# Performance work log

Measured on AMD Instinct MI355X. Metric: run time of the kernel, lower is better.

## Reference

```python
import jax, jax.numpy as jnp
import numpy as np

B, N, C = 2, 4096, 512
NUM_HEADS = 8
HEAD_DIM = C // NUM_HEADS
SCALE = HEAD_DIM ** -0.5
THETA = 10000.0


def setup_inputs() -> dict:
    key = jax.random.key(0)
    ks = jax.random.split(key, 5)
    x = jax.random.normal(ks[0], (B, N, C), dtype=jnp.float32)
    Wqkv = jax.random.normal(ks[1], (3 * C, C), dtype=jnp.float32) * 0.02
    bqkv = jax.random.normal(ks[2], (3 * C,), dtype=jnp.float32) * 0.02
    Wproj = jax.random.normal(ks[3], (C, C), dtype=jnp.float32) * 0.02
    bproj = jax.random.normal(ks[4], (C,), dtype=jnp.float32) * 0.02
    return {"x": x, "Wqkv": Wqkv, "bqkv": bqkv, "Wproj": Wproj, "bproj": bproj}


def _rope(x, seq_len, head_dim):
    # x: [B, H, N, head_dim]; interleaved rotary embedding
    freqs = 1.0 / THETA ** (jnp.arange(0, head_dim, 2, dtype=jnp.float32) / head_dim)  # [hd/2]
    t = jnp.arange(seq_len, dtype=jnp.float32)
    freqs_cis = jnp.outer(t, freqs)                      # [N, hd/2]
    sin_f = jnp.sin(freqs_cis)
    cos_f = jnp.cos(freqs_cis)
    x_even = x[..., ::2]                                 # [B, H, N, hd/2]
    x_odd = x[..., 1::2]
    rot = jnp.stack(
        [x_even * cos_f - x_odd * sin_f,
         x_even * sin_f + x_odd * cos_f],
        axis=-1,
    )                                                    # [B, H, N, hd/2, 2]
    return rot.reshape(x.shape)


def reference(x, Wqkv, bqkv, Wproj, bproj):
    b, n, c = x.shape
    # fused QKV projection: y = x @ W.T + b
    qkv = x @ Wqkv.T + bqkv                              # [B, N, 3C]
    qkv = qkv.reshape(b, n, 3, NUM_HEADS, HEAD_DIM)
    qkv = jnp.transpose(qkv, (2, 0, 3, 1, 4))            # [3, B, H, N, hd]
    q, k, v = qkv[0], qkv[1], qkv[2]
    q = _rope(q, n, HEAD_DIM)
    k = _rope(k, n, HEAD_DIM)
    attn = jnp.einsum('bhqd,bhkd->bhqk', q, k) * SCALE   # [B, H, N, N]
    attn = jax.nn.softmax(attn, axis=-1)
    out = jnp.einsum('bhqk,bhkd->bhqd', attn, v)         # [B, H, N, hd]
    out = jnp.transpose(out, (0, 2, 1, 3)).reshape(b, n, c)
    return out @ Wproj.T + bproj
```

## Files before the change

### kernel.cpp

```cpp
#include <hip/hip_runtime.h>
#include <hip/hip_bf16.h>
#include <stdint.h>

#define B_ 2
#define N_ 4096
#define C_ 512
#define H_ 8
#define D_ 64
#define M_ (B_*N_)
#define K3_ (3*C_)
#define NCH 2

typedef __attribute__((ext_vector_type(8)))  short short8;
typedef __attribute__((ext_vector_type(4)))  float f32x4;
typedef __attribute__((ext_vector_type(16))) float f32x16;

static __device__ __forceinline__ unsigned short f2bf(float f) {
  union { float f; unsigned u; } cv; cv.f = f;
  unsigned r = cv.u + 0x7fffu + ((cv.u >> 16) & 1u);
  return (unsigned short)(r >> 16);
}
static __device__ __forceinline__ float bf2f(short x) {
  union { unsigned u; float f; } cv;
  cv.u = ((unsigned)(unsigned short)x) << 16;
  return cv.f;
}
static __device__ __forceinline__ float fexp2(float x) {
#if __has_builtin(__builtin_amdgcn_exp2f)
  return __builtin_amdgcn_exp2f(x);
#else
  return exp2f(x);
#endif
}
static __device__ __forceinline__ unsigned cvt_pk_bf16(float a, float b) {
  unsigned r;
  asm("v_cvt_pk_bf16_f32 %0, %1, %2" : "=v"(r) : "v"(a), "v"(b));
  return r;
}
static __device__ __forceinline__ void gload_lds16(const void* g, void* l) {
  __builtin_amdgcn_global_load_lds((const __attribute__((address_space(1))) unsigned*)g,
                                   (__attribute__((address_space(3))) unsigned*)l, 16, 0, 0);
}
static __device__ __forceinline__ f32x16 zero16() {
  f32x16 z;
#pragma unroll
  for (int i = 0; i < 16; i++) z[i] = 0.f;
  return z;
}

__global__ void prep(const float* __restrict__ x, const float* __restrict__ Wqkv,
                     const float* __restrict__ Wproj,
                     short* __restrict__ xb, short* __restrict__ wqkvb,
                     short* __restrict__ wprjb, float2* __restrict__ tab) {
  int blk = blockIdx.x, t = threadIdx.x;
  if (blk < 4096) {
    int i = blk * 256 + t;
    float4 v = ((const float4*)x)[i];
    short4 o;
    o.x = (short)f2bf(v.x); o.y = (short)f2bf(v.y);
    o.z = (short)f2bf(v.z); o.w = (short)f2bf(v.w);
    ((short4*)xb)[i] = o;
  } else if (blk < 4864) {
    int i = (blk - 4096) * 256 + t;
    float4 v = ((const float4*)Wqkv)[i];
    short4 o;
    o.x = (short)f2bf(v.x); o.y = (short)f2bf(v.y);
    o.z = (short)f2bf(v.z); o.w = (short)f2bf(v.w);
    ((short4*)wqkvb)[i] = o;
  } else if (blk < 5120) {
    int i = (blk - 4864) * 256 + t;
    float4 v = ((const float4*)Wproj)[i];
    short4 o;
    o.x = (short)f2bf(v.x); o.y = (short)f2bf(v.y);
    o.z = (short)f2bf(v.z); o.w = (short)f2bf(v.w);
    ((short4*)wprjb)[i] = o;
  } else {
    int i = (blk - 5120) * 256 + t;
    int p = i & 31, n = i >> 5;
    float freq = exp2f(-((float)(2 * p) / 64.0f) * 13.287712379549449f);
    float ang = (float)n * freq;
    float s, c;
    sincosf(ang, &s, &c);
    float2 r; r.x = c; r.y = s;
    tab[i] = r;
  }
}

__global__ void rope_vt(const short* __restrict__ qkvb, const float2* __restrict__ tab,
                        short* __restrict__ Qf, short* __restrict__ Kf,
                        short* __restrict__ Vf) {
  __shared__ short tile[128][72];
  int blk = blockIdx.x, t = threadIdx.x;
  if (blk < 1024) {
    int tk = blk >> 9;
    int bh = (blk & 511) >> 5;
    int nb4 = blk & 31;
    int b = bh >> 3, h = bh & 7;
    int n0 = nb4 * 128;
#pragma unroll
    for (int pass = 0; pass < 4; pass++) {
      int row = pass * 32 + (t >> 3), chunk = t & 7;
      short8 v = *(const short8*)(qkvb + (size_t)(b * N_ + n0 + row) * K3_ + tk * C_ + h * D_ + chunk * 8);
      *(short8*)&tile[row][chunk * 8] = v;
    }
    __syncthreads();
    int lane = t & 63, f = t >> 6;
    int c = lane & 31, hi = lane >> 5;
    int d0 = f * 16 + hi * 8;
    float sc = (tk == 0) ? 0.18033688011112042f : 1.0f;
    short* base = (tk ? Kf : Qf);
#pragma unroll
    for (int i = 0; i < 4; i++) {
      int n_l = i * 32 + c;
      short8 v = *(const short8*)&tile[n_l][d0];
      const float2* tp = tab + (size_t)(n0 + n_l) * 32 + (d0 >> 1);
      short8 w;
#pragma unroll
      for (int j = 0; j < 4; j++) {
        float e = bf2f(v[2 * j]), o = bf2f(v[2 * j + 1]);
        float2 cs = tp[j];
        float e2 = (e * cs.x - o * cs.y) * sc;
        float o2 = (e * cs.y + o * cs.x) * sc;
        w[2 * j] = (short)f2bf(e2);
        w[2 * j + 1] = (short)f2bf(o2);
      }
      short* dst = base + (((size_t)(bh * 128 + nb4 * 4 + i) * 4 + f) * 512) + lane * 8;
      *(short8*)dst = w;
    }
  } else {
    int blk2 = blk - 1024;
    int bh = blk2 >> 7, kblk = blk2 & 127;
    int b = bh >> 3, h = bh & 7;
    int n0 = kblk * 32;
    {
      int row = t >> 3, c8 = t & 7;
      short8 v = *(const short8*)(qkvb + (size_t)(b * N_ + n0 + row) * K3_ + 2 * C_ + h * D_ + c8 * 8);
      *(short8*)&tile[row][c8 * 8] = v;
    }
    __syncthreads();
    {
      int frag = t >> 6, lane = t & 63;
      int hi = lane >> 5, c = lane & 31;
      int g = frag & 1, dblk = frag >> 1;
      short8 w;
#pragma unroll
      for (int j = 0; j < 8; j++) w[j] = tile[g * 16 + hi * 8 + j][dblk * 32 + c];
      *(short8*)(Vf + ((size_t)(bh * 128 + kblk) * 4 + frag) * 512 + lane * 8) = w;
    }
  }
}

template<int OUTF32>
__global__ __launch_bounds__(256) void gemm_bt(const short* __restrict__ A, const short* __restrict__ Bw,
                                               const float* __restrict__ bias, void* __restrict__ Cout,
                                               int M, int Nout, int K) {
  __shared__ short As[128 * 32];
  __shared__ short Bs[128 * 32];
  int t = threadIdx.x, lane = t & 63, w = t >> 6, wr = w >> 1, wc = w & 1;
  int tM = blockIdx.x * 128, tN = blockIdx.y * 128;
  int lrow = lane & 15, lhi = lane >> 4;
  f32x4 acc[4][4];
#pragma unroll
  for (int fm = 0; fm < 4; fm++)
#pragma unroll
    for (int fn = 0; fn < 4; fn++)
#pragma unroll
      for (int r = 0; r < 4; r++) acc[fm][fn][r] = 0.f;

  int srow = t >> 2, sq = (t & 3) * 8;
  const short* Ag0 = A  + (size_t)(tM + srow) * K + sq;
  const short* Ag1 = A  + (size_t)(tM + 64 + srow) * K + sq;
  const short* Bg0 = Bw + (size_t)(tN + srow) * K + sq;
  const short* Bg1 = Bw + (size_t)(tN + 64 + srow) * K + sq;
  short* Al0 = As + t * 8;          short* Al1 = As + 2048 + t * 8;
  short* Bl0 = Bs + t * 8;          short* Bl1 = Bs + 2048 + t * 8;

  for (int k0 = 0; k0 < K; k0 += 32) {
    gload_lds16(Ag0 + k0, Al0);
    gload_lds16(Ag1 + k0, Al1);
    gload_lds16(Bg0 + k0, Bl0);
    gload_lds16(Bg1 + k0, Bl1);
    __syncthreads();
    short8 af[4], bfr[4];
#pragma unroll
    for (int f = 0; f < 4; f++) {
      af[f]  = *(const short8*)(As + (wr * 64 + f * 16 + lrow) * 32 + lhi * 8);
      bfr[f] = *(const short8*)(Bs + (wc * 64 + f * 16 + lrow) * 32 + lhi * 8);
    }
#pragma unroll
    for (int fm = 0; fm < 4; fm++)
#pragma unroll
      for (int fn = 0; fn < 4; fn++)
        acc[fm][fn] = __builtin_amdgcn_mfma_f32_16x16x32_bf16(af[fm], bfr[fn], acc[fm][fn], 0, 0, 0);
    __syncthreads();
  }

#pragma unroll
  for (int fn = 0; fn < 4; fn++) {
    int col = tN + wc * 64 + fn * 16 + lrow;
    float bv = bias[col];
#pragma unroll
    for (int fm = 0; fm < 4; fm++) {
      int row0 = tM + wr * 64 + fm * 16 + lhi * 4;
#pragma unroll
      for (int r = 0; r < 4; r++) {
        float v = acc[fm][fn][r] + bv;
        if (OUTF32) ((float*)Cout)[(size_t)(row0 + r) * Nout + col] = v;
        else        ((short*)Cout)[(size_t)(row0 + r) * Nout + col] = (short)f2bf(v);
      }
    }
  }
}

static __device__ __forceinline__ void ld4(short8* dst, const short* p) {
#pragma unroll
  for (int f = 0; f < 4; f++) dst[f] = *(const short8*)(p + f * 512);
}
static __device__ __forceinline__ f32x16 qk4(const short8* k, const short8* q, const f32x16& z0) {
  __builtin_amdgcn_s_setprio(1);
  f32x16 st = __builtin_amdgcn_mfma_f32_32x32x16_bf16(k[0], q[0], z0, 0, 0, 0);
  st = __builtin_amdgcn_mfma_f32_32x32x16_bf16(k[1], q[1], st, 0, 0, 0);
  st = __builtin_amdgcn_mfma_f32_32x32x16_bf16(k[2], q[2], st, 0, 0, 0);
  st = __builtin_amdgcn_mfma_f32_32x32x16_bf16(k[3], q[3], st, 0, 0, 0);
  __builtin_amdgcn_s_setprio(0);
  return st;
}
static __device__ __forceinline__ void soft_pv(const f32x16& st, const short8* v,
                                               f32x16& o0, f32x16& o1, float& lsum) {
  float ls = 0.f;
  unsigned cpk[8];
#pragma unroll
  for (int q2 = 0; q2 < 4; q2++) {
    float e0 = fexp2(st[4 * q2]),     e1 = fexp2(st[4 * q2 + 1]);
    float e2 = fexp2(st[4 * q2 + 2]), e3 = fexp2(st[4 * q2 + 3]);
    ls += (e0 + e1) + (e2 + e3);
    cpk[2 * q2]     = cvt_pk_bf16(e0, e1);
    cpk[2 * q2 + 1] = cvt_pk_bf16(e2, e3);
  }
  lsum += ls;
  unsigned w00 = cpk[0], w02 = cpk[2];
  asm volatile("v_permlane32_swap_b32 %0, %1" : "+v"(w00), "+v"(w02));
  unsigned w01 = cpk[1], w03 = cpk[3];
  asm volatile("v_permlane32_swap_b32 %0, %1" : "+v"(w01), "+v"(w03));
  unsigned w10 = cpk[4], w12 = cpk[6];
  asm volatile("v_permlane32_swap_b32 %0, %1" : "+v"(w10), "+v"(w12));
  unsigned w11 = cpk[5], w13 = cpk[7];
  asm volatile("v_permlane32_swap_b32 %0, %1" : "+v"(w11), "+v"(w13));
  union { unsigned u[4]; short8 s; } u0, u1;
  u0.u[0] = w00; u0.u[1] = w01; u0.u[2] = w02; u0.u[3] = w03;
  u1.u[0] = w10; u1.u[1] = w11; u1.u[2] = w12; u1.u[3] = w13;
  __builtin_amdgcn_s_setprio(1);
  o0 = __builtin_amdgcn_mfma_f32_32x32x16_bf16(u0.s, v[0], o0, 0, 0, 0);
  o0 = __builtin_amdgcn_mfma_f32_32x32x16_bf16(u1.s, v[1], o0, 0, 0, 0);
  o1 = __builtin_amdgcn_mfma_f32_32x32x16_bf16(u0.s, v[2], o1, 0, 0, 0);
  o1 = __builtin_amdgcn_mfma_f32_32x32x16_bf16(u1.s, v[3], o1, 0, 0, 0);
  __builtin_amdgcn_s_setprio(0);
}

__global__ __launch_bounds__(256, 4) void attn(const short* __restrict__ Qf, const short* __restrict__ Kf,
                                               const short* __restrict__ Vf,
                                               short* __restrict__ Op, float* __restrict__ lp) {
  __shared__ short Ks[2][2048];
  __shared__ short Vs[2][2048];
  int bh = blockIdx.x;
  int ch = blockIdx.z;
  int t = threadIdx.x;
  int wv = t >> 6, lane = t & 63;
  int c = lane & 31, hi = lane >> 5;
  int q0 = blockIdx.y * 128 + wv * 32;
  const int nkb = N_ / (NCH * 32);
  int kb0 = ch * nkb;

  const short* Qb = Qf + ((size_t)(bh * 128 + (q0 >> 5)) * 4) * 512 + lane * 8;
  const short* Kg = Kf + ((size_t)(bh * 128 + kb0) * 4) * 512 + t * 8;
  const short* Vg = Vf + ((size_t)(bh * 128 + kb0) * 4) * 512 + t * 8;

  short8 qf4[4];
  ld4(qf4, Qb);

  const f32x16 z0 = zero16();
  f32x16 o0 = z0, o1 = z0;
  float lsum = 0.f;

  gload_lds16(Kg, &Ks[0][t * 8]);
  gload_lds16(Vg, &Vs[0][t * 8]);
  __syncthreads();

  int buf = 0;
  for (int it = 0; it < nkb; ++it) {
    if (it + 1 < nkb) {
      gload_lds16(Kg + (size_t)(it + 1) * 2048, &Ks[buf ^ 1][t * 8]);
      gload_lds16(Vg + (size_t)(it + 1) * 2048, &Vs[buf ^ 1][t * 8]);
    }
    short8 kf[4], vf[4];
#pragma unroll
    for (int f = 0; f < 4; f++) kf[f] = *(const short8*)&Ks[buf][f * 512 + lane * 8];
#pragma unroll
    for (int f = 0; f < 4; f++) vf[f] = *(const short8*)&Vs[buf][f * 512 + lane * 8];
    f32x16 st = qk4(kf, qf4, z0);
    soft_pv(st, vf, o0, o1, lsum);
    __syncthreads();
    buf ^= 1;
  }

  float lt = lsum + __shfl_xor(lsum, 32);
  if (hi == 0) lp[((size_t)ch * 16 + bh) * N_ + q0 + c] = lt;
  short* obase = Op + ((size_t)ch * 16 + bh) * N_ * D_;
#pragma unroll
  for (int r = 0; r < 16; r++) {
    int ql = (r & 3) + 8 * (r >> 2) + 4 * hi;
    int n = q0 + ql;
    obase[(size_t)n * D_ + c]      = (short)f2bf(o0[r]);
    obase[(size_t)n * D_ + 32 + c] = (short)f2bf(o1[r]);
  }
}

__global__ void combine(const short* __restrict__ Op, const float* __restrict__ lp,
                        short* __restrict__ AO) {
  int i = blockIdx.x * blockDim.x + threadIdx.x;
  if (i >= 16 * N_ * 8) return;
  int d8 = i & 7, q = (i >> 3) & (N_ - 1), bh = i >> 15;
  const size_t chs = (size_t)16 * N_ * D_;
  size_t base = ((size_t)bh * N_ + q) * D_ + d8 * 8;
  float acc[8];
#pragma unroll
  for (int j = 0; j < 8; j++) acc[j] = 0.f;
  float l = 0.f;
#pragma unroll
  for (int chv = 0; chv < NCH; chv++) {
    short8 v = *(const short8*)(Op + chv * chs + base);
#pragma unroll
    for (int j = 0; j < 8; j++) acc[j] += bf2f(v[j]);
    l += lp[((size_t)chv * 16 + bh) * N_ + q];
  }
  float inv = 1.0f / l;
  int bb = bh >> 3, h = bh & 7;
  short8 o;
#pragma unroll
  for (int j = 0; j < 8; j++) o[j] = (short)f2bf(acc[j] * inv);
  *(short8*)(AO + ((size_t)(bb * N_ + q)) * C_ + h * D_ + d8 * 8) = o;
}

extern "C" void kernel_launch(void* const* d_in, const int* in_sizes, int n_in,
                              void* d_out, int out_size, void* d_ws, size_t ws_size,
                              hipStream_t stream) {
  const float* x     = (const float*)d_in[0];
  const float* Wqkv  = (const float*)d_in[1];
  const float* bqkv  = (const float*)d_in[2];
  const float* Wproj = (const float*)d_in[3];
  const float* bproj = (const float*)d_in[4];
  float* out = (float*)d_out;
  char* ws = (char*)d_ws;

  const size_t off_wprjb = 0;
  const size_t off_tab   = 524288;
  const size_t off_q     = 1572864;
  const size_t off_k     = 9961472;
  const size_t off_vt    = 18350080;
  const size_t off_ao    = 26738688;
  const size_t off_xb    = 35127296;
  const size_t off_wqkvb = 43515904;
  const size_t off_qkvb  = 45088768;
  const size_t off_op    = 35127296;
  const size_t off_l     = 68681728;
  if (ws_size < 70254592) return;

  short* xb    = (short*)(ws + off_xb);
  short* wqkvb = (short*)(ws + off_wqkvb);
  short* wprjb = (short*)(ws + off_wprjb);
  short* qkvb  = (short*)(ws + off_qkvb);
  short* Qfp   = (short*)(ws + off_q);
  short* Kfp   = (short*)(ws + off_k);
  short* Vfp   = (short*)(ws + off_vt);
  short* AOp   = (short*)(ws + off_ao);
  float2* tab  = (float2*)(ws + off_tab);
  short* Opp   = (short*)(ws + off_op);
  float* lpp   = (float*)(ws + off_l);

  prep<<<dim3(5632), dim3(256), 0, stream>>>(x, Wqkv, Wproj, xb, wqkvb, wprjb, tab);

  gemm_bt<0><<<dim3(64, 12), dim3(256), 0, stream>>>(xb, wqkvb, bqkv, qkvb, M_, K3_, C_);

  rope_vt<<<dim3(3072), dim3(256), 0, stream>>>(qkvb, tab, Qfp, Kfp, Vfp);

  attn<<<dim3(16, 32, NCH), dim3(256), 0, stream>>>(Qfp, Kfp, Vfp, Opp, lpp);
  combine<<<dim3(2048), dim3(256), 0, stream>>>(Opp, lpp, AOp);

  gemm_bt<1><<<dim3(64, 4), dim3(256), 0, stream>>>(AOp, wprjb, bproj, (void*)out, M_, C_, C_);
}
```

Before: 143.6 us.

## Widen GEMM K-tile with XOR-swizzled LDS, ones-MFMA row sums, 64-key attention steps

The GEMM now stages 64-wide K tiles with an XOR swizzle to avoid LDS bank conflicts. It is templated on M fragments so the output projection uses 64-row tiles and twice as many blocks. The attention kernel processes two 32-key sub-blocks per barrier, halving synchronization count. It also computes softmax row sums via an extra MFMA against a ones vector instead of VALU adds, which changes summation precision to bf16-rounded probabilities and uses more LDS and registers.

```diff
diff --git a/kernel.cpp b/kernel.cpp
--- a/kernel.cpp
+++ b/kernel.cpp
@@ -150,48 +150,51 @@
   }
 }
 
-template<int OUTF32>
+template<int OUTF32, int MFR>
 __global__ __launch_bounds__(256) void gemm_bt(const short* __restrict__ A, const short* __restrict__ Bw,
                                                const float* __restrict__ bias, void* __restrict__ Cout,
                                                int M, int Nout, int K) {
-  __shared__ short As[128 * 32];
-  __shared__ short Bs[128 * 32];
+  __shared__ short As[MFR * 32 * 64];
+  __shared__ short Bs[128 * 64];
   int t = threadIdx.x, lane = t & 63, w = t >> 6, wr = w >> 1, wc = w & 1;
-  int tM = blockIdx.x * 128, tN = blockIdx.y * 128;
+  int tM = blockIdx.x * (MFR * 32), tN = blockIdx.y * 128;
   int lrow = lane & 15, lhi = lane >> 4;
-  f32x4 acc[4][4];
-#pragma unroll
-  for (int fm = 0; fm < 4; fm++)
+  int rs = (lrow & 7) * 8;
+  f32x4 acc[MFR][4];
+#pragma unroll
+  for (int fm = 0; fm < MFR; fm++)
 #pragma unroll
     for (int fn = 0; fn < 4; fn++)
 #pragma unroll
       for (int r = 0; r < 4; r++) acc[fm][fn][r] = 0.f;
 
-  int srow = t >> 2, sq = (t & 3) * 8;
-  const short* Ag0 = A  + (size_t)(tM + srow) * K + sq;
-  const short* Ag1 = A  + (size_t)(tM + 64 + srow) * K + sq;
-  const short* Bg0 = Bw + (size_t)(tN + srow) * K + sq;
-  const short* Bg1 = Bw + (size_t)(tN + 64 + srow) * K + sq;
-  short* Al0 = As + t * 8;          short* Al1 = As + 2048 + t * 8;
-  short* Bl0 = Bs + t * 8;          short* Bl1 = Bs + 2048 + t * 8;
-
-  for (int k0 = 0; k0 < K; k0 += 32) {
-    gload_lds16(Ag0 + k0, Al0);
-    gload_lds16(Ag1 + k0, Al1);
-    gload_lds16(Bg0 + k0, Bl0);
-    gload_lds16(Bg1 + k0, Bl1);
+  int srow = t >> 3;
+  int sq = ((t & 7) * 8) ^ ((srow & 7) * 8);
+
+  for (int k0 = 0; k0 < K; k0 += 64) {
+#pragma unroll
+    for (int p = 0; p < MFR; p++)
+      gload_lds16(A + (size_t)(tM + p * 32 + srow) * K + k0 + sq, As + p * 2048 + t * 8);
+#pragma unroll
+    for (int p = 0; p < 4; p++)
+      gload_lds16(Bw + (size_t)(tN + p * 32 + srow) * K + k0 + sq, Bs + p * 2048 + t * 8);
     __syncthreads();
-    short8 af[4], bfr[4];
-#pragma unroll
-    for (int f = 0; f < 4; f++) {
-      af[f]  = *(const short8*)(As + (wr * 64 + f * 16 + lrow) * 32 + lhi * 8);
-      bfr[f] = *(const short8*)(Bs + (wc * 64 + f * 16 + lrow) * 32 + lhi * 8);
-    }
-#pragma unroll
-    for (int fm = 0; fm < 4; fm++)
-#pragma unroll
-      for (int fn = 0; fn < 4; fn++)
-        acc[fm][fn] = __builtin_amdgcn_mfma_f32_16x16x32_bf16(af[fm], bfr[fn], acc[fm][fn], 0, 0, 0);
+#pragma unroll
+    for (int kk = 0; kk < 2; kk++) {
+      int ko = (kk * 32 + lhi * 8) ^ rs;
+      short8 af[MFR], bfr[4];
+#pragma unroll
+      for (int f = 0; f < MFR; f++)
+        af[f] = *(const short8*)(As + (wr * (MFR * 16) + f * 16 + lrow) * 64 + ko);
+#pragma unroll
+      for (int f = 0; f < 4; f++)
+        bfr[f] = *(const short8*)(Bs + (wc * 64 + f * 16 + lrow) * 64 + ko);
+#pragma unroll
+      for (int fm = 0; fm < MFR; fm++)
+#pragma unroll
+        for (int fn = 0; fn < 4; fn++)
+          acc[fm][fn] = __builtin_amdgcn_mfma_f32_16x16x32_bf16(af[fm], bfr[fn], acc[fm][fn], 0, 0, 0);
+    }
     __syncthreads();
   }
 
@@ -200,8 +203,8 @@
     int col = tN + wc * 64 + fn * 16 + lrow;
     float bv = bias[col];
 #pragma unroll
-    for (int fm = 0; fm < 4; fm++) {
-      int row0 = tM + wr * 64 + fm * 16 + lhi * 4;
+    for (int fm = 0; fm < MFR; fm++) {
+      int row0 = tM + wr * (MFR * 16) + fm * 16 + lhi * 4;
 #pragma unroll
       for (int r = 0; r < 4; r++) {
         float v = acc[fm][fn][r] + bv;
@@ -212,10 +215,6 @@
   }
 }
 
-static __device__ __forceinline__ void ld4(short8* dst, const short* p) {
-#pragma unroll
-  for (int f = 0; f < 4; f++) dst[f] = *(const short8*)(p + f * 512);
-}
 static __device__ __forceinline__ f32x16 qk4(const short8* k, const short8* q, const f32x16& z0) {
   __builtin_amdgcn_s_setprio(1);
   f32x16 st = __builtin_amdgcn_mfma_f32_32x32x16_bf16(k[0], q[0], z0, 0, 0, 0);
@@ -225,19 +224,16 @@
   __builtin_amdgcn_s_setprio(0);
   return st;
 }
-static __device__ __forceinline__ void soft_pv(const f32x16& st, const short8* v,
-                                               f32x16& o0, f32x16& o1, float& lsum) {
-  float ls = 0.f;
+static __device__ __forceinline__ void soft_pv(const f32x16& st, const short8* v, const short8& ones,
+                                               f32x16& o0, f32x16& o1, f32x16& o2) {
   unsigned cpk[8];
 #pragma unroll
   for (int q2 = 0; q2 < 4; q2++) {
     float e0 = fexp2(st[4 * q2]),     e1 = fexp2(st[4 * q2 + 1]);
     float e2 = fexp2(st[4 * q2 + 2]), e3 = fexp2(st[4 * q2 + 3]);
-    ls += (e0 + e1) + (e2 + e3);
     cpk[2 * q2]     = cvt_pk_bf16(e0, e1);
     cpk[2 * q2 + 1] = cvt_pk_bf16(e2, e3);
   }
-  lsum += ls;
   unsigned w00 = cpk[0], w02 = cpk[2];
   asm volatile("v_permlane32_swap_b32 %0, %1" : "+v"(w00), "+v"(w02));
   unsigned w01 = cpk[1], w03 = cpk[3];
@@ -254,57 +250,75 @@
   o0 = __builtin_amdgcn_mfma_f32_32x32x16_bf16(u1.s, v[1], o0, 0, 0, 0);
   o1 = __builtin_amdgcn_mfma_f32_32x32x16_bf16(u0.s, v[2], o1, 0, 0, 0);
   o1 = __builtin_amdgcn_mfma_f32_32x32x16_bf16(u1.s, v[3], o1, 0, 0, 0);
+  o2 = __builtin_amdgcn_mfma_f32_32x32x16_bf16(u0.s, ones, o2, 0, 0, 0);
+  o2 = __builtin_amdgcn_mfma_f32_32x32x16_bf16(u1.s, ones, o2, 0, 0, 0);
   __builtin_amdgcn_s_setprio(0);
 }
 
 __global__ __launch_bounds__(256, 4) void attn(const short* __restrict__ Qf, const short* __restrict__ Kf,
                                                const short* __restrict__ Vf,
                                                short* __restrict__ Op, float* __restrict__ lp) {
-  __shared__ short Ks[2][2048];
-  __shared__ short Vs[2][2048];
+  __shared__ short Ks[2][4096];
+  __shared__ short Vs[2][4096];
   int bh = blockIdx.x;
   int ch = blockIdx.z;
   int t = threadIdx.x;
   int wv = t >> 6, lane = t & 63;
   int c = lane & 31, hi = lane >> 5;
   int q0 = blockIdx.y * 128 + wv * 32;
-  const int nkb = N_ / (NCH * 32);
-  int kb0 = ch * nkb;
+  const int nkb2 = N_ / (NCH * 64);
+  int kb0 = ch * (N_ / (NCH * 32));
 
   const short* Qb = Qf + ((size_t)(bh * 128 + (q0 >> 5)) * 4) * 512 + lane * 8;
   const short* Kg = Kf + ((size_t)(bh * 128 + kb0) * 4) * 512 + t * 8;
   const short* Vg = Vf + ((size_t)(bh * 128 + kb0) * 4) * 512 + t * 8;
 
   short8 qf4[4];
-  ld4(qf4, Qb);
+#pragma unroll
+  for (int f = 0; f < 4; f++) qf4[f] = *(const short8*)(Qb + f * 512);
+
+  short8 ones;
+#pragma unroll
+  for (int j = 0; j < 8; j++) ones[j] = (short)0x3F80;
 
   const f32x16 z0 = zero16();
-  f32x16 o0 = z0, o1 = z0;
-  float lsum = 0.f;
-
-  gload_lds16(Kg, &Ks[0][t * 8]);
-  gload_lds16(Vg, &Vs[0][t * 8]);
+  f32x16 o0 = z0, o1 = z0, o2 = z0;
+
+  gload_lds16(Kg,        &Ks[0][t * 8]);
+  gload_lds16(Kg + 2048, &Ks[0][2048 + t * 8]);
+  gload_lds16(Vg,        &Vs[0][t * 8]);
+  gload_lds16(Vg + 2048, &Vs[0][2048 + t * 8]);
   __syncthreads();
 
   int buf = 0;
-  for (int it = 0; it < nkb; ++it) {
-    if (it + 1 < nkb) {
-      gload_lds16(Kg + (size_t)(it + 1) * 2048, &Ks[buf ^ 1][t * 8]);
-      gload_lds16(Vg + (size_t)(it + 1) * 2048, &Vs[buf ^ 1][t * 8]);
-    }
-    short8 kf[4], vf[4];
-#pragma unroll
-    for (int f = 0; f < 4; f++) kf[f] = *(const short8*)&Ks[buf][f * 512 + lane * 8];
-#pragma unroll
-    for (int f = 0; f < 4; f++) vf[f] = *(const short8*)&Vs[buf][f * 512 + lane * 8];
-    f32x16 st = qk4(kf, qf4, z0);
-    soft_pv(st, vf, o0, o1, lsum);
+  for (int it = 0; it < nkb2; ++it) {
+    if (it + 1 < nkb2) {
+      const short* Kn = Kg + (size_t)(it + 1) * 4096;
+      const short* Vn = Vg + (size_t)(it + 1) * 4096;
+      gload_lds16(Kn,        &Ks[buf ^ 1][t * 8]);
+      gload_lds16(Kn + 2048, &Ks[buf ^ 1][2048 + t * 8]);
+      gload_lds16(Vn,        &Vs[buf ^ 1][t * 8]);
+      gload_lds16(Vn + 2048, &Vs[buf ^ 1][2048 + t * 8]);
+    }
+#pragma unroll
+    for (int s = 0; s < 2; s++) {
+      short8 kf[4], vf[4];
+#pragma unroll
+      for (int f = 0; f < 4; f++) kf[f] = *(const short8*)&Ks[buf][s * 2048 + f * 512 + lane * 8];
+#pragma unroll
+      for (int f = 0; f < 4; f++) vf[f] = *(const short8*)&Vs[buf][s * 2048 + f * 512 + lane * 8];
+      f32x16 st = qk4(kf, qf4, z0);
+      soft_pv(st, vf, ones, o0, o1, o2);
+    }
     __syncthreads();
     buf ^= 1;
   }
 
-  float lt = lsum + __shfl_xor(lsum, 32);
-  if (hi == 0) lp[((size_t)ch * 16 + bh) * N_ + q0 + c] = lt;
+  if (c == 0) {
+    float* lrow = lp + ((size_t)ch * 16 + bh) * N_ + q0;
+#pragma unroll
+    for (int r = 0; r < 16; r++) lrow[(r & 3) + 8 * (r >> 2) + 4 * hi] = o2[r];
+  }
   short* obase = Op + ((size_t)ch * 16 + bh) * N_ * D_;
 #pragma unroll
   for (int r = 0; r < 16; r++) {
@@ -379,12 +393,12 @@
 
   prep<<<dim3(5632), dim3(256), 0, stream>>>(x, Wqkv, Wproj, xb, wqkvb, wprjb, tab);
 
-  gemm_bt<0><<<dim3(64, 12), dim3(256), 0, stream>>>(xb, wqkvb, bqkv, qkvb, M_, K3_, C_);
+  gemm_bt<0, 4><<<dim3(64, 12), dim3(256), 0, stream>>>(xb, wqkvb, bqkv, qkvb, M_, K3_, C_);
 
   rope_vt<<<dim3(3072), dim3(256), 0, stream>>>(qkvb, tab, Qfp, Kfp, Vfp);
 
   attn<<<dim3(16, 32, NCH), dim3(256), 0, stream>>>(Qfp, Kfp, Vfp, Opp, lpp);
   combine<<<dim3(2048), dim3(256), 0, stream>>>(Opp, lpp, AOp);
 
-  gemm_bt<1><<<dim3(64, 4), dim3(256), 0, stream>>>(AOp, wprjb, bproj, (void*)out, M_, C_, C_);
-}
+  gemm_bt<1, 2><<<dim3(128, 4), dim3(256), 0, stream>>>(AOp, wprjb, bproj, (void*)out, M_, C_, C_);
+}
```

New measurement: 141.0 us. About the same (-1.8%).
